# Optimization experiments

Hardware: AMD Instinct MI355X
Metric: run time of the kernel (lower is better)

The kernel has to match this reference:

```python
import jax, jax.numpy as jnp
import numpy as np

NEG_SLOPE = 0.2  # PyG GATConv default negative_slope


def gat_layer(x, src, dst, W, a_src, a_dst, bias, concat, N):
    """PyG GATConv: h = xW; e_ij = LeakyReLU(a_src.h_j + a_dst.h_i);
    alpha = segment-softmax over incoming edges of i; out_i = sum_j alpha_ij h_j."""
    H, C = a_src.shape
    h = (x @ W).reshape(N, H, C)                      # [N,H,C]
    alpha_s = jnp.einsum('nhc,hc->nh', h, a_src)      # [N,H]
    alpha_d = jnp.einsum('nhc,hc->nh', h, a_dst)      # [N,H]
    e = jax.nn.leaky_relu(alpha_s[src] + alpha_d[dst], NEG_SLOPE)  # [E,H]
    # numerically-stable segment softmax over destination nodes
    m = jax.ops.segment_max(e, dst, num_segments=N)   # [N,H]
    e = jnp.exp(e - m[dst])
    denom = jax.ops.segment_sum(e, dst, num_segments=N)
    alpha = e / (denom[dst] + 1e-16)                  # [E,H]
    msg = h[src] * alpha[:, :, None]                  # [E,H,C]
    out = jax.ops.segment_sum(msg, dst, num_segments=N)  # [N,H,C]
    out = out.reshape(N, H * C) if concat else out.mean(axis=1)
    return out + bias


def setup_inputs() -> dict:
    key = jax.random.key(0)
    ks = jax.random.split(key, 12)
    N, E, F_IN, C, H = 50000, 800000, 512, 32, 8
    s = 0.05
    x = jax.random.normal(ks[0], (N, F_IN), dtype=jnp.float32)
    edge_index = jax.random.randint(ks[1], (2, E), 0, N, dtype=jnp.int64)
    W1 = jax.random.normal(ks[2], (F_IN, H * C), dtype=jnp.float32) * s
    as1 = jax.random.normal(ks[3], (H, C), dtype=jnp.float32) * s
    ad1 = jax.random.normal(ks[4], (H, C), dtype=jnp.float32) * s
    b1 = jnp.zeros((H * C,), dtype=jnp.float32)
    W2 = jax.random.normal(ks[5], (H * C, H * C), dtype=jnp.float32) * s
    as2 = jax.random.normal(ks[6], (H, C), dtype=jnp.float32) * s
    ad2 = jax.random.normal(ks[7], (H, C), dtype=jnp.float32) * s
    b2 = jnp.zeros((C,), dtype=jnp.float32)
    Wp = jax.random.normal(ks[8], (C, 1), dtype=jnp.float32) * s
    bp = jnp.zeros((1,), dtype=jnp.float32)
    return {"edge_index": edge_index, "x": x, "W1": W1, "as1": as1, "ad1": ad1,
            "b1": b1, "W2": W2, "as2": as2, "ad2": ad2, "b2": b2,
            "Wp": Wp, "bp": bp}


def reference(edge_index, x, W1, as1, ad1, b1, W2, as2, ad2, b2, Wp, bp):
    N = x.shape[0]
    # PyG GATConv adds self-loops by default
    loops = jnp.arange(N, dtype=edge_index.dtype)
    src = jnp.concatenate([edge_index[0], loops])
    dst = jnp.concatenate([edge_index[1], loops])
    h = gat_layer(x, src, dst, W1, as1, ad1, b1, concat=True, N=N)
    h = jax.nn.relu(h)
    # F.dropout(training=self.training) is identity in eval mode
    h = gat_layer(h, src, dst, W2, as2, ad2, b2, concat=False, N=N)
    return jax.nn.sigmoid(h @ Wp + bp)   # [N,1]
```

## Files before the change

### kernel.cpp

```cpp
#include <hip/hip_runtime.h>
#include <math.h>

#define H_HEADS 8
#define C_DIM   32
#define HC      256
#define F_IN    512
#define NEG_SLOPE 0.2f

typedef __attribute__((ext_vector_type(8))) short    bf16x8;
typedef __attribute__((ext_vector_type(4))) short    s16x4;
typedef __attribute__((ext_vector_type(4))) float    f32x4;
typedef __attribute__((ext_vector_type(2))) float    f32x2;
typedef __attribute__((ext_vector_type(8))) _Float16 h16x8;

__device__ __forceinline__ short f2bf(float f) {
    union { float f; unsigned u; } v; v.f = f;
    unsigned r = v.u + 0x7FFF + ((v.u >> 16) & 1);
    return (short)(r >> 16);
}

__device__ __forceinline__ void gl2lds16(const short* g, short* l) {
    __builtin_amdgcn_global_load_lds(
        (const __attribute__((address_space(1))) void*)g,
        (__attribute__((address_space(3))) void*)l, 16, 0, 0);
}

__global__ void wfrag_kernel(const float* __restrict__ W, short* __restrict__ Wf, int K)
{
    int tid = blockIdx.x * 256 + threadIdx.x;
    if (tid >= K * HC) return;
    int j  = tid & 7;
    int l  = (tid >> 3) & 63;
    int nb = (tid >> 9) & 15;
    int s  = tid >> 13;
    int k  = s * 32 + (l >> 4) * 8 + j;
    int n  = nb * 16 + (l & 15);
    Wf[tid] = f2bf(W[(size_t)k * HC + n]);
}

__global__ __launch_bounds__(256) void gemm1_mfma(const float* __restrict__ A32,
    const short* __restrict__ Bf, unsigned char* __restrict__ h8,
    const float* __restrict__ a_s, const float* __restrict__ a_d,
    float* __restrict__ alpha_s, float* __restrict__ alpha_d, int M)
{
    __shared__ short Bs[2][8192];

    const int tid  = threadIdx.x;
    const int w    = tid >> 6;
    const int lane = tid & 63;
    const int quad = lane >> 4;
    const int ml   = lane & 15;
    const int bm   = blockIdx.x * 64;

    const int rowA = bm + w * 16 + ml;
    const int rowL = rowA < M ? rowA : M - 1;

    f32x4 acc[16];
    #pragma unroll
    for (int nb = 0; nb < 16; ++nb) acc[nb] = (f32x4){0.f, 0.f, 0.f, 0.f};

    const int nsteps = F_IN >> 5;

    {
        const short* g = Bf + (size_t)w * 2048 + lane * 8;
        short* l = &Bs[0][w * 2048];
        #pragma unroll
        for (int c = 0; c < 4; ++c) gl2lds16(g + c * 512, l + c * 512);
    }

    const float* abase = A32 + (size_t)rowL * F_IN + quad * 8;
    float4 pa[2][2];
    pa[0][0] = *(const float4*)(abase);
    pa[0][1] = *(const float4*)(abase + 4);
    pa[1][0] = *(const float4*)(abase + 32);
    pa[1][1] = *(const float4*)(abase + 36);

    for (int s = 0; s < nsteps; ++s) {
        __syncthreads();

        if (s + 1 < nsteps) {
            const short* g = Bf + (size_t)(s + 1) * 8192 + w * 2048 + lane * 8;
            short* l = &Bs[(s + 1) & 1][w * 2048];
            #pragma unroll
            for (int c = 0; c < 4; ++c) gl2lds16(g + c * 512, l + c * 512);
        }

        bf16x8 af;
        {
            float4 q0 = pa[s & 1][0], q1 = pa[s & 1][1];
            af[0] = f2bf(q0.x); af[1] = f2bf(q0.y); af[2] = f2bf(q0.z); af[3] = f2bf(q0.w);
            af[4] = f2bf(q1.x); af[5] = f2bf(q1.y); af[6] = f2bf(q1.z); af[7] = f2bf(q1.w);
        }
        if (s + 2 < nsteps) {
            pa[s & 1][0] = *(const float4*)(abase + (s + 2) * 32);
            pa[s & 1][1] = *(const float4*)(abase + (s + 2) * 32 + 4);
        }

        const short* bsrc = &Bs[s & 1][lane * 8];
        #pragma unroll
        for (int nb = 0; nb < 16; ++nb) {
            bf16x8 bfr = *(const bf16x8*)(bsrc + nb * 512);
            acc[nb] = __builtin_amdgcn_mfma_f32_16x16x32_bf16(af, bfr, acc[nb], 0, 0, 0);
        }
    }

    float as_v[16], ad_v[16];
    #pragma unroll
    for (int nb = 0; nb < 16; ++nb) {
        as_v[nb] = a_s[nb * 16 + ml];
        ad_v[nb] = a_d[nb * 16 + ml];
    }

    __syncthreads();
    float* Als = (float*)&Bs[0][0];
    float* Ald = Als + 512;

    #pragma unroll
    for (int r = 0; r < 4; ++r) {
        const int rl  = w * 16 + quad * 4 + r;
        const int row = bm + rl;

        if (row < M) {
            unsigned char* hrow = h8 + (size_t)row * HC;
            #pragma unroll
            for (int i = 0; i < 8; ++i) {
                int pk = __builtin_amdgcn_cvt_pk_fp8_f32(acc[2 * i][r], acc[2 * i + 1][r], 0, false);
                hrow[(2 * i) * 16 + ml]     = (unsigned char)(pk & 0xFF);
                hrow[(2 * i + 1) * 16 + ml] = (unsigned char)((pk >> 8) & 0xFF);
            }
        }

        float hs[8], hd[8];
        #pragma unroll
        for (int q = 0; q < 8; ++q) {
            hs[q] = acc[2 * q][r] * as_v[2 * q] + acc[2 * q + 1][r] * as_v[2 * q + 1];
            hd[q] = acc[2 * q][r] * ad_v[2 * q] + acc[2 * q + 1][r] * ad_v[2 * q + 1];
        }
        #pragma unroll
        for (int off = 1; off < 16; off <<= 1) {
            #pragma unroll
            for (int q = 0; q < 8; ++q) {
                hs[q] += __shfl_xor(hs[q], off);
                hd[q] += __shfl_xor(hd[q], off);
            }
        }
        if (ml == 0) {
            #pragma unroll
            for (int q = 0; q < 8; ++q) {
                Als[rl * 8 + q] = hs[q];
                Ald[rl * 8 + q] = hd[q];
            }
        }
    }
    __syncthreads();
    #pragma unroll
    for (int k = 0; k < 2; ++k) {
        int idx = tid + k * 256;
        int rl = idx >> 3, q = idx & 7;
        int row = bm + rl;
        if (row < M) {
            alpha_s[(size_t)row * H_HEADS + q] = Als[idx];
            alpha_d[(size_t)row * H_HEADS + q] = Ald[idx];
        }
    }
}

__global__ __launch_bounds__(256) void gemm2_persist(const short* __restrict__ z1b,
    const short* __restrict__ Bf2, unsigned char* __restrict__ h8,
    const float* __restrict__ a_s, const float* __restrict__ a_d,
    float* __restrict__ alpha_s, float* __restrict__ alpha_d, int M)
{
    __shared__ short Bs[32768];

    const int tid  = threadIdx.x;
    const int w    = tid >> 6;
    const int lane = tid & 63;
    const int quad = lane >> 4;
    const int ml   = lane & 15;
    const int ch   = blockIdx.x & 1;
    const int bid2 = blockIdx.x >> 1;
    const int bstr = gridDim.x >> 1;

    #pragma unroll
    for (int s = 0; s < 8; ++s) {
        const short* gbase = Bf2 + (size_t)(s * 16 + ch * 8) * 512;
        #pragma unroll
        for (int sw = 0; sw < 2; ++sw) {
            int i = sw * 2048 + tid * 8;
            gl2lds16(gbase + i, &Bs[s * 4096 + i]);
        }
    }
    __syncthreads();

    float as_v[8], ad_v[8];
    #pragma unroll
    for (int nb = 0; nb < 8; ++nb) {
        as_v[nb] = a_s[(ch * 8 + nb) * 16 + ml];
        ad_v[nb] = a_d[(ch * 8 + nb) * 16 + ml];
    }

    const int nt = (M + 63) >> 6;
    for (int rt = bid2; rt < nt; rt += bstr) {
        const int rowA = rt * 64 + w * 16 + ml;
        const int rowL = rowA < M ? rowA : M - 1;
        const short* arow = z1b + (size_t)rowL * HC;

        bf16x8 av[8];
        #pragma unroll
        for (int s = 0; s < 8; ++s)
            av[s] = *(const bf16x8*)(arow + s * 32 + quad * 8);

        f32x4 acc[8];
        #pragma unroll
        for (int nb = 0; nb < 8; ++nb) acc[nb] = (f32x4){0.f, 0.f, 0.f, 0.f};

        #pragma unroll
        for (int s = 0; s < 8; ++s) {
            const short* bsrc = &Bs[s * 4096 + lane * 8];
            #pragma unroll
            for (int nb = 0; nb < 8; ++nb) {
                bf16x8 bfr = *(const bf16x8*)(bsrc + nb * 512);
                acc[nb] = __builtin_amdgcn_mfma_f32_16x16x32_bf16(av[s], bfr, acc[nb], 0, 0, 0);
            }
        }

        #pragma unroll
        for (int r = 0; r < 4; ++r) {
            const int row = rt * 64 + w * 16 + quad * 4 + r;
            float hs[4], hd[4];
            #pragma unroll
            for (int q = 0; q < 4; ++q) {
                hs[q] = acc[2 * q][r] * as_v[2 * q] + acc[2 * q + 1][r] * as_v[2 * q + 1];
                hd[q] = acc[2 * q][r] * ad_v[2 * q] + acc[2 * q + 1][r] * ad_v[2 * q + 1];
            }
            #pragma unroll
            for (int off = 1; off < 16; off <<= 1) {
                #pragma unroll
                for (int q = 0; q < 4; ++q) {
                    hs[q] += __shfl_xor(hs[q], off);
                    hd[q] += __shfl_xor(hd[q], off);
                }
            }
            if (row < M) {
                unsigned char* hrow = h8 + (size_t)row * HC;
                #pragma unroll
                for (int i = 0; i < 4; ++i) {
                    int pk = __builtin_amdgcn_cvt_pk_fp8_f32(acc[2 * i][r], acc[2 * i + 1][r], 0, false);
                    hrow[(ch * 8 + 2 * i) * 16 + ml]     = (unsigned char)(pk & 0xFF);
                    hrow[(ch * 8 + 2 * i + 1) * 16 + ml] = (unsigned char)((pk >> 8) & 0xFF);
                }
                if (ml == 0) {
                    #pragma unroll
                    for (int q = 0; q < 4; ++q) {
                        alpha_s[(size_t)row * H_HEADS + ch * 4 + q] = hs[q];
                        alpha_d[(size_t)row * H_HEADS + ch * 4 + q] = hd[q];
                    }
                }
            }
        }
    }
}

__global__ __launch_bounds__(256) void wcalc_kernel(const int2* __restrict__ es,
    const float* __restrict__ alpha_s, const float* __restrict__ alpha_d,
    _Float16* __restrict__ wq, int P)
{
    int p = blockIdx.x * 256 + threadIdx.x;
    if (p >= P) return;
    int2 sd = es[p];
    const float4* as = (const float4*)(alpha_s + (size_t)sd.x * H_HEADS);
    const float4* ad = (const float4*)(alpha_d + (size_t)sd.y * H_HEADS);
    float4 s0 = as[0], s1 = as[1], d0 = ad[0], d1 = ad[1];
    float e[8] = {s0.x + d0.x, s0.y + d0.y, s0.z + d0.z, s0.w + d0.w,
                  s1.x + d1.x, s1.y + d1.y, s1.z + d1.z, s1.w + d1.w};
    h16x8 o;
    #pragma unroll
    for (int h = 0; h < 8; ++h) {
        float v = e[h] > 0.f ? e[h] : NEG_SLOPE * e[h];
        o[h] = (_Float16)__expf(v);
    }
    *(h16x8*)(wq + (size_t)p * H_HEADS) = o;
}

__global__ void zero_int(int* __restrict__ p, int n)
{
    int i = blockIdx.x * 256 + threadIdx.x;
    if (i < n) p[i] = 0;
}

__global__ void hist_kernel(const int* __restrict__ ei, int E, int N,
                            int* __restrict__ cnt)
{
    int e = blockIdx.x * 256 + threadIdx.x;
    if (e < E) atomicAdd(&cnt[ei[E + e]], 1);
    else if (e < E + N) atomicAdd(&cnt[e - E], 1);
}

__global__ __launch_bounds__(256) void scan_sum(const int* __restrict__ cnt, int n,
                                                int* __restrict__ chunk_sum)
{
    __shared__ int lds[256];
    int b = blockIdx.x, t = threadIdx.x;
    int base = b * 1024 + t * 4;
    int s = 0;
    #pragma unroll
    for (int j = 0; j < 4; ++j) { int i = base + j; if (i < n) s += cnt[i]; }
    lds[t] = s; __syncthreads();
    for (int off = 128; off > 0; off >>= 1) {
        if (t < off) lds[t] += lds[t + off];
        __syncthreads();
    }
    if (t == 0) chunk_sum[b] = lds[0];
}

__global__ void scan_top(const int* __restrict__ chunk_sum, int nch,
                         int* __restrict__ chunk_off, int* __restrict__ row_ptr,
                         int n_nodes)
{
    int t = threadIdx.x;
    int v = (t < nch) ? chunk_sum[t] : 0;
    int inc = v;
    #pragma unroll
    for (int off = 1; off < 64; off <<= 1) {
        int u = __shfl_up(inc, off);
        if (t >= off) inc += u;
    }
    if (t < nch) chunk_off[t] = inc - v;
    if (t == 63) row_ptr[n_nodes] = inc;
}

__global__ __launch_bounds__(256) void scan_local(const int* __restrict__ cnt, int n,
    const int* __restrict__ chunk_off, int* __restrict__ row_ptr)
{
    __shared__ int lds[256];
    int b = blockIdx.x, t = threadIdx.x;
    int base = b * 1024 + t * 4;
    int v[4]; int s = 0;
    #pragma unroll
    for (int j = 0; j < 4; ++j) { int i = base + j; v[j] = (i < n) ? cnt[i] : 0; s += v[j]; }
    lds[t] = s; __syncthreads();
    for (int off = 1; off < 256; off <<= 1) {
        int u = (t >= off) ? lds[t - off] : 0;
        __syncthreads();
        lds[t] += u;
        __syncthreads();
    }
    int run = lds[t] - s + chunk_off[b];
    #pragma unroll
    for (int j = 0; j < 4; ++j) {
        int i = base + j;
        if (i < n) row_ptr[i] = run;
        run += v[j];
    }
}

#define SC_T 8192
__global__ __launch_bounds__(256) void scatter1_kernel(const int* __restrict__ ei,
    int E, int ET, int NBK, const int* __restrict__ row_ptr,
    int* __restrict__ fill1, int2* __restrict__ tmp)
{
    __shared__ int hist[1024];
    const int t  = threadIdx.x;
    const int e0 = blockIdx.x * SC_T;

    for (int b = t; b < NBK; b += 256) hist[b] = 0;
    __syncthreads();

    #pragma unroll 4
    for (int k = 0; k < SC_T / 256; ++k) {
        int e = e0 + k * 256 + t;
        if (e < ET) {
            int dst = (e < E) ? ei[E + e] : e - E;
            atomicAdd(&hist[dst >> 6], 1);
        }
    }
    __syncthreads();

    for (int b = t; b < NBK; b += 256) {
        int c = hist[b];
        int base = 0;
        if (c > 0) base = row_ptr[b << 6] + atomicAdd(&fill1[b], c);
        __syncthreads();
        hist[b] = base;
        __syncthreads();
    }
    __syncthreads();

    #pragma unroll 4
    for (int k = 0; k < SC_T / 256; ++k) {
        int e = e0 + k * 256 + t;
        if (e < ET) {
            int src, dst;
            if (e < E) { src = ei[e]; dst = ei[E + e]; }
            else       { src = dst = e - E; }
            int pos = atomicAdd(&hist[dst >> 6], 1);
            tmp[pos] = make_int2(src, dst);
        }
    }
}

__global__ __launch_bounds__(256) void scatter2_kernel(const int2* __restrict__ tmp,
    const int* __restrict__ row_ptr, int N, int2* __restrict__ es)
{
    __shared__ int f[64];
    int b = blockIdx.x;
    int n0 = b * 64;
    int n1 = n0 + 64; if (n1 > N) n1 = N;
    if (threadIdx.x < 64) f[threadIdx.x] = 0;
    __syncthreads();
    int p0 = row_ptr[n0], p1 = row_ptr[n1];
    for (int p = p0 + threadIdx.x; p < p1; p += 256) {
        int2 sd = tmp[p];
        int pos = row_ptr[sd.y] + atomicAdd(&f[sd.y & 63], 1);
        es[pos] = sd;
    }
}

__global__ __launch_bounds__(256) void agg1_kernel(const unsigned* __restrict__ h8,
    const _Float16* __restrict__ wq, const int* __restrict__ row_ptr,
    const int2* __restrict__ es, const float* __restrict__ bias,
    short* __restrict__ z_bf, int N)
{
    const int l = threadIdx.x & 63;
    const int i = blockIdx.x * 4 + (threadIdx.x >> 6);
    if (i >= N) return;
    const int hh = l >> 3;
    const int beg = row_ptr[i], end = row_ptr[i + 1];
    f32x4 acc = {0.f, 0.f, 0.f, 0.f};
    float dsum = 0.f;
    int p = beg;
    for (; p + 7 < end; p += 8) {
        int s[8]; float w[8]; unsigned hv[8];
        #pragma unroll
        for (int u = 0; u < 8; ++u) s[u] = es[p + u].x;
        #pragma unroll
        for (int u = 0; u < 8; ++u) w[u] = (float)wq[(size_t)(p + u) * 8 + hh];
        #pragma unroll
        for (int u = 0; u < 8; ++u) hv[u] = h8[(size_t)s[u] * 64 + l];
        #pragma unroll
        for (int u = 0; u < 8; ++u) {
            f32x2 lo = __builtin_amdgcn_cvt_pk_f32_fp8(hv[u], false);
            f32x2 hi = __builtin_amdgcn_cvt_pk_f32_fp8(hv[u], true);
            acc[0] = fmaf(w[u], lo[0], acc[0]);
            acc[1] = fmaf(w[u], lo[1], acc[1]);
            acc[2] = fmaf(w[u], hi[0], acc[2]);
            acc[3] = fmaf(w[u], hi[1], acc[3]);
            dsum += w[u];
        }
    }
    for (; p < end; ++p) {
        int s0 = es[p].x;
        float w0 = (float)wq[(size_t)p * 8 + hh];
        unsigned hv = h8[(size_t)s0 * 64 + l];
        f32x2 lo = __builtin_amdgcn_cvt_pk_f32_fp8(hv, false);
        f32x2 hi = __builtin_amdgcn_cvt_pk_f32_fp8(hv, true);
        acc[0] = fmaf(w0, lo[0], acc[0]);
        acc[1] = fmaf(w0, lo[1], acc[1]);
        acc[2] = fmaf(w0, hi[0], acc[2]);
        acc[3] = fmaf(w0, hi[1], acc[3]);
        dsum += w0;
    }
    float inv = 1.f / (dsum + 1e-16f);
    s16x4 pk;
    #pragma unroll
    for (int j = 0; j < 4; ++j) {
        float z = acc[j] * inv + bias[4 * l + j];
        pk[j] = f2bf(z > 0.f ? z : 0.f);
    }
    *(s16x4*)(z_bf + (size_t)i * HC + 4 * l) = pk;
}

__global__ __launch_bounds__(256) void agg2_kernel(const unsigned* __restrict__ h8,
    const _Float16* __restrict__ wq, const int* __restrict__ row_ptr,
    const int2* __restrict__ es, const float* __restrict__ b2,
    const float* __restrict__ Wp, const float* __restrict__ bp,
    float* __restrict__ out, int N)
{
    const int l = threadIdx.x & 63;
    const int i = blockIdx.x * 4 + (threadIdx.x >> 6);
    if (i >= N) return;
    const int hh = l >> 3;
    const int beg = row_ptr[i], end = row_ptr[i + 1];
    f32x4 acc = {0.f, 0.f, 0.f, 0.f};
    float dsum = 0.f;
    int p = beg;
    for (; p + 7 < end; p += 8) {
        int s[8]; float w[8]; unsigned hv[8];
        #pragma unroll
        for (int u = 0; u < 8; ++u) s[u] = es[p + u].x;
        #pragma unroll
        for (int u = 0; u < 8; ++u) w[u] = (float)wq[(size_t)(p + u) * 8 + hh];
        #pragma unroll
        for (int u = 0; u < 8; ++u) hv[u] = h8[(size_t)s[u] * 64 + l];
        #pragma unroll
        for (int u = 0; u < 8; ++u) {
            f32x2 lo = __builtin_amdgcn_cvt_pk_f32_fp8(hv[u], false);
            f32x2 hi = __builtin_amdgcn_cvt_pk_f32_fp8(hv[u], true);
            acc[0] = fmaf(w[u], lo[0], acc[0]);
            acc[1] = fmaf(w[u], lo[1], acc[1]);
            acc[2] = fmaf(w[u], hi[0], acc[2]);
            acc[3] = fmaf(w[u], hi[1], acc[3]);
            dsum += w[u];
        }
    }
    for (; p < end; ++p) {
        int s0 = es[p].x;
        float w0 = (float)wq[(size_t)p * 8 + hh];
        unsigned hv = h8[(size_t)s0 * 64 + l];
        f32x2 lo = __builtin_amdgcn_cvt_pk_f32_fp8(hv, false);
        f32x2 hi = __builtin_amdgcn_cvt_pk_f32_fp8(hv, true);
        acc[0] = fmaf(w0, lo[0], acc[0]);
        acc[1] = fmaf(w0, lo[1], acc[1]);
        acc[2] = fmaf(w0, hi[0], acc[2]);
        acc[3] = fmaf(w0, hi[1], acc[3]);
        dsum += w0;
    }
    float inv = 1.f / (dsum + 1e-16f);
    int cc = (4 * l) & 31;
    float partial = 0.f;
    #pragma unroll
    for (int j = 0; j < 4; ++j) partial = fmaf(acc[j] * inv, Wp[cc + j], partial);
    if (l < 8) {
        #pragma unroll
        for (int j = 0; j < 4; ++j) partial = fmaf(8.f * b2[4 * l + j], Wp[4 * l + j], partial);
    }
    #pragma unroll
    for (int off = 32; off > 0; off >>= 1) partial += __shfl_xor(partial, off);
    if (l == 0) out[i] = 1.f / (1.f + __expf(-(0.125f * partial + bp[0])));
}

extern "C" void kernel_launch(void* const* d_in, const int* in_sizes, int n_in,
                              void* d_out, int out_size, void* d_ws, size_t ws_size,
                              hipStream_t stream)
{
    const int*   ei  = (const int*)d_in[0];
    const float* x   = (const float*)d_in[1];
    const float* W1  = (const float*)d_in[2];
    const float* as1 = (const float*)d_in[3];
    const float* ad1 = (const float*)d_in[4];
    const float* b1  = (const float*)d_in[5];
    const float* W2  = (const float*)d_in[6];
    const float* as2 = (const float*)d_in[7];
    const float* ad2 = (const float*)d_in[8];
    const float* b2  = (const float*)d_in[9];
    const float* Wp  = (const float*)d_in[10];
    const float* bp  = (const float*)d_in[11];
    float* out = (float*)d_out;

    const int E   = in_sizes[0] / 2;
    const int N   = in_sizes[1] / F_IN;
    const int ET  = E + N;
    const int NBK = (N + 63) / 64;

    float*         asb = (float*)d_ws;
    float*         adb = asb + (size_t)N * H_HEADS;
    unsigned char* h8  = (unsigned char*)(adb + (size_t)N * H_HEADS);
    short*         z1b = (short*)(h8 + (size_t)N * HC);
    short*         Wf1 = z1b + (size_t)N * HC;
    short*         Wf2 = Wf1 + (size_t)F_IN * HC;
    _Float16*      wq  = (_Float16*)(Wf2 + (size_t)HC * HC);
    int2*          es  = (int2*)(wq + (size_t)ET * H_HEADS);
    int2*          tmp = es + ET;
    int* cnt       = (int*)(tmp + ET);
    int* fill1     = cnt + N;
    int* row_ptr   = fill1 + NBK;
    int* chunk_off = row_ptr + N + 1;
    int* chunk_sum = chunk_off + 64;

    const int NCH = (N + 1023) / 1024;
    const int MB  = (N + 63) / 64;
    const int NB4 = (N + 3) / 4;
    const int NB1 = (ET + SC_T - 1) / SC_T;

    zero_int<<<(N + NBK + 255) / 256, 256, 0, stream>>>(cnt, N + NBK);
    hist_kernel<<<(ET + 255) / 256, 256, 0, stream>>>(ei, E, N, cnt);
    scan_sum<<<NCH, 256, 0, stream>>>(cnt, N, chunk_sum);
    scan_top<<<1, 64, 0, stream>>>(chunk_sum, NCH, chunk_off, row_ptr, N);
    scan_local<<<NCH, 256, 0, stream>>>(cnt, N, chunk_off, row_ptr);
    scatter1_kernel<<<NB1, 256, 0, stream>>>(ei, E, ET, NBK, row_ptr, fill1, tmp);
    scatter2_kernel<<<NBK, 256, 0, stream>>>(tmp, row_ptr, N, es);

    wfrag_kernel<<<(F_IN * HC + 255) / 256, 256, 0, stream>>>(W1, Wf1, F_IN);
    wfrag_kernel<<<(HC * HC + 255) / 256, 256, 0, stream>>>(W2, Wf2, HC);

    gemm1_mfma<<<MB, 256, 0, stream>>>(x, Wf1, h8, as1, ad1, asb, adb, N);
    wcalc_kernel<<<(ET + 255) / 256, 256, 0, stream>>>(es, asb, adb, wq, ET);
    agg1_kernel<<<NB4, 256, 0, stream>>>((const unsigned*)h8, wq, row_ptr, es, b1, z1b, N);

    gemm2_persist<<<512, 256, 0, stream>>>(z1b, Wf2, h8, as2, ad2, asb, adb, N);
    wcalc_kernel<<<(ET + 255) / 256, 256, 0, stream>>>(es, asb, adb, wq, ET);
    agg2_kernel<<<NB4, 256, 0, stream>>>((const unsigned*)h8, wq, row_ptr, es, b2, Wp, bp, out, N);
}
```

Measured before the change: 431.6 us.

## Double gemm1 row tile to 128 rows per block to reuse B fragments

The first-layer GEMM kernel now computes two 64-row sub-tiles per block. Each B fragment read from LDS feeds two MFMAs, which halves B traffic per output and halves the number of blocks. The cost is twice the accumulator registers (32 f32x4), lower occupancy, and fewer blocks to spread across the CUs for N=50000. The LDS scratch for the alpha values grows to 1024 floats each, which still fits in the existing 2x8192-short buffer.

```diff
diff --git a/kernel.cpp b/kernel.cpp
--- a/kernel.cpp
+++ b/kernel.cpp
@@ -50,14 +50,20 @@
     const int lane = tid & 63;
     const int quad = lane >> 4;
     const int ml   = lane & 15;
-    const int bm   = blockIdx.x * 64;
-
-    const int rowA = bm + w * 16 + ml;
-    const int rowL = rowA < M ? rowA : M - 1;
-
-    f32x4 acc[16];
-    #pragma unroll
-    for (int nb = 0; nb < 16; ++nb) acc[nb] = (f32x4){0.f, 0.f, 0.f, 0.f};
+    const int bm   = blockIdx.x * 128;
+
+    int rowL[2];
+    #pragma unroll
+    for (int rs = 0; rs < 2; ++rs) {
+        int r = bm + rs * 64 + w * 16 + ml;
+        rowL[rs] = r < M ? r : M - 1;
+    }
+
+    f32x4 acc[2][16];
+    #pragma unroll
+    for (int rs = 0; rs < 2; ++rs)
+        #pragma unroll
+        for (int nb = 0; nb < 16; ++nb) acc[rs][nb] = (f32x4){0.f, 0.f, 0.f, 0.f};
 
     const int nsteps = F_IN >> 5;
 
@@ -68,12 +74,16 @@
         for (int c = 0; c < 4; ++c) gl2lds16(g + c * 512, l + c * 512);
     }
 
-    const float* abase = A32 + (size_t)rowL * F_IN + quad * 8;
-    float4 pa[2][2];
-    pa[0][0] = *(const float4*)(abase);
-    pa[0][1] = *(const float4*)(abase + 4);
-    pa[1][0] = *(const float4*)(abase + 32);
-    pa[1][1] = *(const float4*)(abase + 36);
+    const float* ab[2] = { A32 + (size_t)rowL[0] * F_IN + quad * 8,
+                           A32 + (size_t)rowL[1] * F_IN + quad * 8 };
+    float4 pa[2][2][2];
+    #pragma unroll
+    for (int rs = 0; rs < 2; ++rs) {
+        pa[0][rs][0] = *(const float4*)(ab[rs]);
+        pa[0][rs][1] = *(const float4*)(ab[rs] + 4);
+        pa[1][rs][0] = *(const float4*)(ab[rs] + 32);
+        pa[1][rs][1] = *(const float4*)(ab[rs] + 36);
+    }
 
     for (int s = 0; s < nsteps; ++s) {
         __syncthreads();
@@ -85,22 +95,29 @@
             for (int c = 0; c < 4; ++c) gl2lds16(g + c * 512, l + c * 512);
         }
 
-        bf16x8 af;
-        {
-            float4 q0 = pa[s & 1][0], q1 = pa[s & 1][1];
-            af[0] = f2bf(q0.x); af[1] = f2bf(q0.y); af[2] = f2bf(q0.z); af[3] = f2bf(q0.w);
-            af[4] = f2bf(q1.x); af[5] = f2bf(q1.y); af[6] = f2bf(q1.z); af[7] = f2bf(q1.w);
+        bf16x8 af[2];
+        #pragma unroll
+        for (int rs = 0; rs < 2; ++rs) {
+            float4 q0 = pa[s & 1][rs][0], q1 = pa[s & 1][rs][1];
+            af[rs][0] = f2bf(q0.x); af[rs][1] = f2bf(q0.y);
+            af[rs][2] = f2bf(q0.z); af[rs][3] = f2bf(q0.w);
+            af[rs][4] = f2bf(q1.x); af[rs][5] = f2bf(q1.y);
+            af[rs][6] = f2bf(q1.z); af[rs][7] = f2bf(q1.w);
         }
         if (s + 2 < nsteps) {
-            pa[s & 1][0] = *(const float4*)(abase + (s + 2) * 32);
-            pa[s & 1][1] = *(const float4*)(abase + (s + 2) * 32 + 4);
+            #pragma unroll
+            for (int rs = 0; rs < 2; ++rs) {
+                pa[s & 1][rs][0] = *(const float4*)(ab[rs] + (s + 2) * 32);
+                pa[s & 1][rs][1] = *(const float4*)(ab[rs] + (s + 2) * 32 + 4);
+            }
         }
 
         const short* bsrc = &Bs[s & 1][lane * 8];
         #pragma unroll
         for (int nb = 0; nb < 16; ++nb) {
             bf16x8 bfr = *(const bf16x8*)(bsrc + nb * 512);
-            acc[nb] = __builtin_amdgcn_mfma_f32_16x16x32_bf16(af, bfr, acc[nb], 0, 0, 0);
+            acc[0][nb] = __builtin_amdgcn_mfma_f32_16x16x32_bf16(af[0], bfr, acc[0][nb], 0, 0, 0);
+            acc[1][nb] = __builtin_amdgcn_mfma_f32_16x16x32_bf16(af[1], bfr, acc[1][nb], 0, 0, 0);
         }
     }
 
@@ -113,48 +130,52 @@
 
     __syncthreads();
     float* Als = (float*)&Bs[0][0];
-    float* Ald = Als + 512;
-
-    #pragma unroll
-    for (int r = 0; r < 4; ++r) {
-        const int rl  = w * 16 + quad * 4 + r;
-        const int row = bm + rl;
-
-        if (row < M) {
-            unsigned char* hrow = h8 + (size_t)row * HC;
-            #pragma unroll
-            for (int i = 0; i < 8; ++i) {
-                int pk = __builtin_amdgcn_cvt_pk_fp8_f32(acc[2 * i][r], acc[2 * i + 1][r], 0, false);
-                hrow[(2 * i) * 16 + ml]     = (unsigned char)(pk & 0xFF);
-                hrow[(2 * i + 1) * 16 + ml] = (unsigned char)((pk >> 8) & 0xFF);
-            }
-        }
-
-        float hs[8], hd[8];
-        #pragma unroll
-        for (int q = 0; q < 8; ++q) {
-            hs[q] = acc[2 * q][r] * as_v[2 * q] + acc[2 * q + 1][r] * as_v[2 * q + 1];
-            hd[q] = acc[2 * q][r] * ad_v[2 * q] + acc[2 * q + 1][r] * ad_v[2 * q + 1];
-        }
-        #pragma unroll
-        for (int off = 1; off < 16; off <<= 1) {
+    float* Ald = Als + 1024;
+
+    #pragma unroll
+    for (int rs = 0; rs < 2; ++rs) {
+        #pragma unroll
+        for (int r = 0; r < 4; ++r) {
+            const int rl  = rs * 64 + w * 16 + quad * 4 + r;
+            const int row = bm + rl;
+
+            if (row < M) {
+                unsigned char* hrow = h8 + (size_t)row * HC;
+                #pragma unroll
+                for (int i = 0; i < 8; ++i) {
+                    int pk = __builtin_amdgcn_cvt_pk_fp8_f32(acc[rs][2 * i][r],
+                                                             acc[rs][2 * i + 1][r], 0, false);
+                    hrow[(2 * i) * 16 + ml]     = (unsigned char)(pk & 0xFF);
+                    hrow[(2 * i + 1) * 16 + ml] = (unsigned char)((pk >> 8) & 0xFF);
+                }
+            }
+
+            float hs[8], hd[8];
             #pragma unroll
             for (int q = 0; q < 8; ++q) {
-                hs[q] += __shfl_xor(hs[q], off);
-                hd[q] += __shfl_xor(hd[q], off);
-            }
-        }
-        if (ml == 0) {
+                hs[q] = acc[rs][2 * q][r] * as_v[2 * q] + acc[rs][2 * q + 1][r] * as_v[2 * q + 1];
+                hd[q] = acc[rs][2 * q][r] * ad_v[2 * q] + acc[rs][2 * q + 1][r] * ad_v[2 * q + 1];
+            }
             #pragma unroll
-            for (int q = 0; q < 8; ++q) {
-                Als[rl * 8 + q] = hs[q];
-                Ald[rl * 8 + q] = hd[q];
+            for (int off = 1; off < 16; off <<= 1) {
+                #pragma unroll
+                for (int q = 0; q < 8; ++q) {
+                    hs[q] += __shfl_xor(hs[q], off);
+                    hd[q] += __shfl_xor(hd[q], off);
+                }
+            }
+            if (ml == 0) {
+                #pragma unroll
+                for (int q = 0; q < 8; ++q) {
+                    Als[rl * 8 + q] = hs[q];
+                    Ald[rl * 8 + q] = hd[q];
+                }
             }
         }
     }
     __syncthreads();
     #pragma unroll
-    for (int k = 0; k < 2; ++k) {
+    for (int k = 0; k < 4; ++k) {
         int idx = tid + k * 256;
         int rl = idx >> 3, q = idx & 7;
         int row = bm + rl;
@@ -568,7 +589,7 @@
     int* chunk_sum = chunk_off + 64;
 
     const int NCH = (N + 1023) / 1024;
-    const int MB  = (N + 63) / 64;
+    const int MB  = (N + 127) / 128;
     const int NB4 = (N + 3) / 4;
     const int NB1 = (ET + SC_T - 1) / SC_T;
 
```

New measurement: 440.9 us. +2.2%, slower.
